# Performance work log

Measured on AMD Instinct MI355X. Metric: run time of the kernel, lower is better.

## Reference

```python
import jax, jax.numpy as jnp
import numpy as np

N, E = 40000, 640000
S_IN, V_IN = 64, 32            # input irreps: 64x0e + 32x1o (dim 160)
S_MID, V_MID = 96, 128         # tp output: (64+32)x0e, (64+32+32)x1o
S_OUT, V_OUT = 96, 32          # gate irreps_in: 64x0e scalars + 32x0e gates + 32x1o gated
R = 64                         # edge scalar (radial basis) dim
FC_HID = 64
W_NUMEL = 64 + 64 + 32 + 32 + 32  # per-edge tp weights ('uvu', v=1): 224
NUM_NEIGHBORS = 16.0


def setup_inputs() -> dict:
    key = jax.random.key(0)
    ks = jax.random.split(key, 13)
    return {
        "node_features": jax.random.normal(ks[0], (N, S_IN + 3 * V_IN), jnp.float32),
        "node_attr": jnp.ones((N, 1), jnp.float32),
        "edge_src": jax.random.randint(ks[1], (E,), 0, N),
        "edge_dst": jax.random.randint(ks[2], (E,), 0, N),
        "edge_attr": jax.random.normal(ks[3], (E, 4), jnp.float32),
        "edge_scalars": jax.random.normal(ks[4], (E, R), jnp.float32),
        "lin1_ws": jax.random.normal(ks[5], (S_IN, S_IN), jnp.float32),
        "lin1_wv": jax.random.normal(ks[6], (V_IN, V_IN), jnp.float32),
        "fc_w1": jax.random.normal(ks[7], (R, FC_HID), jnp.float32),
        "fc_w2": jax.random.normal(ks[8], (FC_HID, W_NUMEL), jnp.float32),
        "sc_ws": jax.random.normal(ks[9], (S_IN, S_OUT), jnp.float32),
        "sc_wv": jax.random.normal(ks[10], (V_IN, V_OUT), jnp.float32),
        "lin2_ws": jax.random.normal(ks[11], (S_MID, S_OUT), jnp.float32),
        "lin2_wv": jax.random.normal(ks[12], (V_MID, V_OUT), jnp.float32),
    }


def _inv(d):
    return 1.0 / jnp.sqrt(jnp.float32(d))


def _forward(node_features, node_attr, edge_attr, edge_scalars,
             lin1_ws, lin1_wv, fc_w1, fc_w2, sc_ws, sc_wv, lin2_ws, lin2_wv,
             edge_src, edge_dst):
    n = node_features.shape[0]
    s = node_features[:, :S_IN]                      # [N,64] 0e
    v = node_features[:, S_IN:].reshape(n, V_IN, 3)  # [N,32,3] 1o
    a = node_attr                                    # [N,1] scalar node attr

    # self-connection: FullyConnectedTensorProduct(input, 1x0e attr, out) == per-irrep linear
    sc_s = (s @ sc_ws) * a * _inv(S_IN)                                    # [N,96]
    sc_v = jnp.einsum('nci,cd->ndi', v, sc_wv) * a[:, :, None] * _inv(V_IN)  # [N,32,3]

    # lin1
    h_s = (s @ lin1_ws) * a * _inv(S_IN)
    h_v = jnp.einsum('nci,cd->ndi', v, lin1_wv) * a[:, :, None] * _inv(V_IN)

    # per-edge tensor-product weights from FC on edge scalars (silu MLP, no bias)
    hid = jax.nn.silu((edge_scalars @ fc_w1) * _inv(R))
    w = (hid @ fc_w2) * _inv(FC_HID)                 # [E,224]
    w1, w2, w3, w4, w5 = jnp.split(w, [64, 128, 160, 192], axis=-1)

    # gather source node features
    es = h_s[edge_src]                               # [E,64]
    ev = h_v[edge_src]                               # [E,32,3]
    e0 = edge_attr[:, :1]                            # [E,1]  0e
    e1 = edge_attr[:, 1:4]                           # [E,3]  1o

    # Clebsch-Gordan tensor product paths ('uvu', per-edge weights)
    m_s1 = w1 * es * e0                                                   # 0e x 0e -> 0e [E,64]
    m_s2 = w4 * jnp.einsum('eci,ei->ec', ev, e1) * _inv(3)                # 1o x 1o -> 0e [E,32]
    m_v1 = (w2 * es)[:, :, None] * e1[:, None, :]                         # 0e x 1o -> 1o [E,64,3]
    m_v2 = w3[:, :, None] * ev * e0[:, :, None]                           # 1o x 0e -> 1o [E,32,3]
    m_v3 = w5[:, :, None] * jnp.cross(ev, e1[:, None, :]) * _inv(2)       # 1o x 1o -> 1o [E,32,3]

    mid_s = jnp.concatenate([m_s1, m_s2], axis=-1)        # [E,96]
    mid_v = jnp.concatenate([m_v1, m_v2, m_v3], axis=1)   # [E,128,3]

    # scatter-sum to destination nodes, normalized by sqrt(num_neighbors)
    inv_nn = 1.0 / jnp.sqrt(jnp.float32(NUM_NEIGHBORS))
    agg_s = jax.ops.segment_sum(mid_s, edge_dst, num_segments=n) * inv_nn
    agg_v = jax.ops.segment_sum(mid_v, edge_dst, num_segments=n) * inv_nn

    # lin2
    o_s = (agg_s @ lin2_ws) * a * _inv(S_MID)                                  # [N,96]
    o_v = jnp.einsum('nci,cd->ndi', agg_v, lin2_wv) * a[:, :, None] * _inv(V_MID)  # [N,32,3]

    pre_s = sc_s + o_s
    pre_v = sc_v + o_v

    # Gate: silu on scalars, sigmoid gates multiply the l=1 features
    scalars = jax.nn.silu(pre_s[:, :64])
    gates = jax.nn.sigmoid(pre_s[:, 64:96])
    gated = gates[:, :, None] * pre_v                 # [N,32,3]
    return jnp.concatenate([scalars, gated.reshape(n, 3 * V_OUT)], axis=-1)  # [N,160]


def reference(node_features, node_attr, edge_src, edge_dst, edge_attr, edge_scalars,
              lin1_ws, lin1_wv, fc_w1, fc_w2, sc_ws, sc_wv, lin2_ws, lin2_wv):
    return _forward(node_features, node_attr, edge_attr, edge_scalars,
                    lin1_ws, lin1_wv, fc_w1, fc_w2, sc_ws, sc_wv, lin2_ws, lin2_wv,
                    edge_src, edge_dst)
```

## Files before the change

kernel.cpp:

```cpp
#include <hip/hip_runtime.h>

constexpr int N_NODES = 40000;
constexpr int N_EDGES = 640000;

constexpr float C_INV8     = 0.125f;
constexpr float C_INV_S32  = 0.17677669529663687f;
constexpr float C_INV_S3   = 0.57735026918962576f;
constexpr float C_INV_S2   = 0.70710678118654752f;
constexpr float C_INV_S96  = 0.10206207261596575f;
constexpr float C_INV_S128 = 0.08838834764831845f;
constexpr float C_INV_NN   = 0.25f;

typedef __attribute__((ext_vector_type(8))) short short8;
typedef __attribute__((ext_vector_type(4))) float f32x4;

__device__ __forceinline__ unsigned short f2bf(float x) {
  __bf16 b = (__bf16)x;
  return __builtin_bit_cast(unsigned short, b);
}
__device__ __forceinline__ float bf2f(unsigned short h) {
  return __uint_as_float(((unsigned int)h) << 16);
}

__global__ __launch_bounds__(256) void k_prep(
    const float* __restrict__ fc_w1, const float* __restrict__ fc_w2,
    const float* __restrict__ lin2_ws, const float* __restrict__ lin2_wv,
    unsigned short* __restrict__ w1t, unsigned short* __restrict__ w2t,
    unsigned short* __restrict__ wst, unsigned short* __restrict__ wvt)
{
  int t = blockIdx.x * 256 + threadIdx.x;
  if (t < 4096) {
    int c = t >> 6, k = t & 63;
    w1t[c * 64 + k] = f2bf(fc_w1[k * 64 + c]);
  } else if (t < 4096 + 14336) {
    int u = t - 4096; int c = u >> 6, k = u & 63;
    w2t[c * 64 + k] = f2bf(fc_w2[k * 224 + c]);
  } else if (t < 18432 + 9216) {
    int u = t - 18432; int c = u / 96, k = u - c * 96;
    wst[c * 96 + k] = f2bf(lin2_ws[k * 96 + c] * (C_INV_NN * C_INV_S96));
  } else if (t < 27648 + 4096) {
    int u = t - 27648; int d = u >> 7, k = u & 127;
    wvt[d * 128 + k] = f2bf(lin2_wv[k * 32 + d] * (C_INV_NN * C_INV_S128));
  }
}

__global__ __launch_bounds__(256) void k_node_hs(
    const float* __restrict__ nf, const float* __restrict__ attr,
    const float* __restrict__ w, float* __restrict__ h_s)
{
  int t = blockIdx.x * 256 + threadIdx.x;
  if (t >= N_NODES * 64) return;
  int n = t >> 6, c = t & 63;
  const float* s = nf + (long)n * 160;
  float acc = 0.f;
  #pragma unroll 8
  for (int k = 0; k < 64; ++k) acc = fmaf(s[k], w[k * 64 + c], acc);
  h_s[t] = acc * attr[n] * C_INV8;
}

__global__ __launch_bounds__(256) void k_node_hv(
    const float* __restrict__ nf, const float* __restrict__ attr,
    const float* __restrict__ w, float* __restrict__ h_v)
{
  int t = blockIdx.x * 256 + threadIdx.x;
  if (t >= N_NODES * 32) return;
  int n = t >> 5, d = t & 31;
  const float* v = nf + (long)n * 160 + 64;
  float a0 = 0.f, a1 = 0.f, a2 = 0.f;
  #pragma unroll 8
  for (int c = 0; c < 32; ++c) {
    float wv = w[c * 32 + d];
    a0 = fmaf(v[3 * c + 0], wv, a0);
    a1 = fmaf(v[3 * c + 1], wv, a1);
    a2 = fmaf(v[3 * c + 2], wv, a2);
  }
  float sc = attr[n] * C_INV_S32;
  h_v[(long)t * 3 + 0] = a0 * sc;
  h_v[(long)t * 3 + 1] = a1 * sc;
  h_v[(long)t * 3 + 2] = a2 * sc;
}

__global__ __launch_bounds__(256) void k_deg(const int* __restrict__ edst,
                                             int* __restrict__ deg)
{
  int e = blockIdx.x * 256 + threadIdx.x;
  if (e < N_EDGES) atomicAdd(&deg[edst[e]], 1);
}

__global__ __launch_bounds__(1024) void k_scan(const int* __restrict__ deg,
                                               int* __restrict__ start,
                                               int* __restrict__ cursor)
{
  __shared__ int psum[1024];
  int tid = threadIdx.x;
  const int PER = 40;
  int base = tid * PER;
  int s = 0;
  for (int i = 0; i < PER; ++i) {
    int idx = base + i;
    if (idx < N_NODES) s += deg[idx];
  }
  psum[tid] = s;
  __syncthreads();
  for (int off = 1; off < 1024; off <<= 1) {
    int v = psum[tid];
    int u = (tid >= off) ? psum[tid - off] : 0;
    __syncthreads();
    psum[tid] = v + u;
    __syncthreads();
  }
  int run = (tid == 0) ? 0 : psum[tid - 1];
  for (int i = 0; i < PER; ++i) {
    int idx = base + i;
    if (idx < N_NODES) {
      start[idx] = run; cursor[idx] = run;
      run += deg[idx];
    }
  }
  if (tid == 1023) start[N_NODES] = run;
}

__global__ __launch_bounds__(256) void k_fill(const int* __restrict__ edst,
                                              int* __restrict__ cursor,
                                              int* __restrict__ eid)
{
  int e = blockIdx.x * 256 + threadIdx.x;
  if (e < N_EDGES) {
    int p = atomicAdd(&cursor[edst[e]], 1);
    eid[p] = e;
  }
}

__global__ __launch_bounds__(256, 2) void k_edge2(
    const float* __restrict__ escal, const float* __restrict__ eattr,
    const int* __restrict__ esrc,
    const unsigned short* __restrict__ w1t, const unsigned short* __restrict__ w2t,
    const unsigned short* __restrict__ wst, const unsigned short* __restrict__ wvt,
    const float* __restrict__ h_s, const float* __restrict__ h_v,
    unsigned short* __restrict__ e_out)
{
  __shared__ unsigned short hid_lds[64 * 72];
  __shared__ unsigned short w_lds[64 * 232];
  int tid = threadIdx.x, warp = tid >> 6, lane = tid & 63;
  int lr = lane & 15, lg = lane >> 4;
  long e0 = (long)blockIdx.x * 64;
  int r0 = warp * 16;

  long eM = e0 + r0 + lr;
  int srcM = esrc[eM];
  float4 ea4 = *reinterpret_cast<const float4*>(eattr + eM * 4);
  float ea0 = ea4.x, e1x = ea4.y, e1y = ea4.z, e1z = ea4.w;
  float esv[16];
  {
    const float* hsr = h_s + (long)srcM * 64;
    *reinterpret_cast<float4*>(&esv[0])  = *reinterpret_cast<const float4*>(hsr + lg * 8);
    *reinterpret_cast<float4*>(&esv[4])  = *reinterpret_cast<const float4*>(hsr + lg * 8 + 4);
    *reinterpret_cast<float4*>(&esv[8])  = *reinterpret_cast<const float4*>(hsr + 32 + lg * 8);
    *reinterpret_cast<float4*>(&esv[12]) = *reinterpret_cast<const float4*>(hsr + 32 + lg * 8 + 4);
  }
  float evv[24];
  {
    const float* hvr = h_v + (long)srcM * 96 + lg * 24;
    #pragma unroll
    for (int q = 0; q < 6; ++q)
      *reinterpret_cast<float4*>(&evv[4 * q]) = *reinterpret_cast<const float4*>(hvr + 4 * q);
  }

  f32x4 acc[4] = {};
  #pragma unroll
  for (int ks = 0; ks < 2; ++ks) {
    const float* ap = escal + (e0 + r0 + lr) * 64 + ks * 32 + lg * 8;
    float4 a01 = *reinterpret_cast<const float4*>(ap);
    float4 a23 = *reinterpret_cast<const float4*>(ap + 4);
    short8 af;
    af[0] = (short)f2bf(a01.x); af[1] = (short)f2bf(a01.y);
    af[2] = (short)f2bf(a01.z); af[3] = (short)f2bf(a01.w);
    af[4] = (short)f2bf(a23.x); af[5] = (short)f2bf(a23.y);
    af[6] = (short)f2bf(a23.z); af[7] = (short)f2bf(a23.w);
    #pragma unroll
    for (int nt = 0; nt < 4; ++nt) {
      short8 bf = *reinterpret_cast<const short8*>(w1t + (nt * 16 + lr) * 64 + ks * 32 + lg * 8);
      acc[nt] = __builtin_amdgcn_mfma_f32_16x16x32_bf16(af, bf, acc[nt], 0, 0, 0);
    }
  }
  #pragma unroll
  for (int nt = 0; nt < 4; ++nt)
    #pragma unroll
    for (int r = 0; r < 4; ++r) {
      float x = acc[nt][r] * C_INV8;
      float h = x / (1.f + __expf(-x));
      hid_lds[(r0 + lg * 4 + r) * 72 + nt * 16 + lr] = f2bf(h);
    }

  f32x4 acc2[14] = {};
  #pragma unroll
  for (int ks = 0; ks < 2; ++ks) {
    short8 af = *reinterpret_cast<const short8*>(hid_lds + (r0 + lr) * 72 + ks * 32 + lg * 8);
    #pragma unroll
    for (int nt = 0; nt < 14; ++nt) {
      short8 bf = *reinterpret_cast<const short8*>(w2t + (nt * 16 + lr) * 64 + ks * 32 + lg * 8);
      acc2[nt] = __builtin_amdgcn_mfma_f32_16x16x32_bf16(af, bf, acc2[nt], 0, 0, 0);
    }
  }
  #pragma unroll
  for (int nt = 0; nt < 14; ++nt)
    #pragma unroll
    for (int r = 0; r < 4; ++r)
      w_lds[(r0 + lg * 4 + r) * 232 + nt * 16 + lr] = f2bf(acc2[nt][r] * C_INV8);

  const unsigned short* wrow = w_lds + (r0 + lr) * 232;
  short8 w1a = *reinterpret_cast<const short8*>(wrow + lg * 8);
  short8 w1b = *reinterpret_cast<const short8*>(wrow + 32 + lg * 8);
  short8 w2a = *reinterpret_cast<const short8*>(wrow + 64 + lg * 8);
  short8 w2b = *reinterpret_cast<const short8*>(wrow + 96 + lg * 8);
  short8 w3s = *reinterpret_cast<const short8*>(wrow + 128 + lg * 8);
  short8 w4s = *reinterpret_cast<const short8*>(wrow + 160 + lg * 8);
  short8 w5s = *reinterpret_cast<const short8*>(wrow + 192 + lg * 8);

  f32x4 accS[6] = {};
  {
    short8 aS;
    #pragma unroll
    for (int j = 0; j < 8; ++j) aS[j] = (short)f2bf(bf2f((unsigned short)w1a[j]) * esv[j] * ea0);
    #pragma unroll
    for (int nt = 0; nt < 6; ++nt) {
      short8 b = *reinterpret_cast<const short8*>(wst + (nt * 16 + lr) * 96 + lg * 8);
      accS[nt] = __builtin_amdgcn_mfma_f32_16x16x32_bf16(aS, b, accS[nt], 0, 0, 0);
    }
    #pragma unroll
    for (int j = 0; j < 8; ++j) aS[j] = (short)f2bf(bf2f((unsigned short)w1b[j]) * esv[8 + j] * ea0);
    #pragma unroll
    for (int nt = 0; nt < 6; ++nt) {
      short8 b = *reinterpret_cast<const short8*>(wst + (nt * 16 + lr) * 96 + 32 + lg * 8);
      accS[nt] = __builtin_amdgcn_mfma_f32_16x16x32_bf16(aS, b, accS[nt], 0, 0, 0);
    }
    #pragma unroll
    for (int j = 0; j < 8; ++j) {
      float dot = evv[3 * j] * e1x + evv[3 * j + 1] * e1y + evv[3 * j + 2] * e1z;
      aS[j] = (short)f2bf(bf2f((unsigned short)w4s[j]) * dot * C_INV_S3);
    }
    #pragma unroll
    for (int nt = 0; nt < 6; ++nt) {
      short8 b = *reinterpret_cast<const short8*>(wst + (nt * 16 + lr) * 96 + 64 + lg * 8);
      accS[nt] = __builtin_amdgcn_mfma_f32_16x16x32_bf16(aS, b, accS[nt], 0, 0, 0);
    }
  }

  f32x4 accV[6] = {};
  #pragma unroll
  for (int i = 0; i < 3; ++i) {
    float e1i = (i == 0) ? e1x : (i == 1) ? e1y : e1z;
    short8 aV;
    #pragma unroll
    for (int j = 0; j < 8; ++j) aV[j] = (short)f2bf(bf2f((unsigned short)w2a[j]) * esv[j] * e1i);
    #pragma unroll
    for (int nt = 0; nt < 2; ++nt) {
      short8 b = *reinterpret_cast<const short8*>(wvt + (nt * 16 + lr) * 128 + lg * 8);
      accV[i * 2 + nt] = __builtin_amdgcn_mfma_f32_16x16x32_bf16(aV, b, accV[i * 2 + nt], 0, 0, 0);
    }
    #pragma unroll
    for (int j = 0; j < 8; ++j) aV[j] = (short)f2bf(bf2f((unsigned short)w2b[j]) * esv[8 + j] * e1i);
    #pragma unroll
    for (int nt = 0; nt < 2; ++nt) {
      short8 b = *reinterpret_cast<const short8*>(wvt + (nt * 16 + lr) * 128 + 32 + lg * 8);
      accV[i * 2 + nt] = __builtin_amdgcn_mfma_f32_16x16x32_bf16(aV, b, accV[i * 2 + nt], 0, 0, 0);
    }
    #pragma unroll
    for (int j = 0; j < 8; ++j) aV[j] = (short)f2bf(bf2f((unsigned short)w3s[j]) * evv[3 * j + i] * ea0);
    #pragma unroll
    for (int nt = 0; nt < 2; ++nt) {
      short8 b = *reinterpret_cast<const short8*>(wvt + (nt * 16 + lr) * 128 + 64 + lg * 8);
      accV[i * 2 + nt] = __builtin_amdgcn_mfma_f32_16x16x32_bf16(aV, b, accV[i * 2 + nt], 0, 0, 0);
    }
    #pragma unroll
    for (int j = 0; j < 8; ++j) {
      float ex = evv[3 * j], ey = evv[3 * j + 1], ez = evv[3 * j + 2];
      float cr = (i == 0) ? (ey * e1z - ez * e1y)
               : (i == 1) ? (ez * e1x - ex * e1z)
                          : (ex * e1y - ey * e1x);
      aV[j] = (short)f2bf(bf2f((unsigned short)w5s[j]) * cr * C_INV_S2);
    }
    #pragma unroll
    for (int nt = 0; nt < 2; ++nt) {
      short8 b = *reinterpret_cast<const short8*>(wvt + (nt * 16 + lr) * 128 + 96 + lg * 8);
      accV[i * 2 + nt] = __builtin_amdgcn_mfma_f32_16x16x32_bf16(aV, b, accV[i * 2 + nt], 0, 0, 0);
    }
  }

  unsigned short* o_lds = w_lds;
  #pragma unroll
  for (int nt = 0; nt < 6; ++nt)
    #pragma unroll
    for (int r = 0; r < 4; ++r)
      o_lds[(r0 + lg * 4 + r) * 232 + nt * 16 + lr] = f2bf(accS[nt][r]);
  #pragma unroll
  for (int q = 0; q < 6; ++q) {
    int i = q >> 1, nt = q & 1;
    #pragma unroll
    for (int r = 0; r < 4; ++r)
      o_lds[(r0 + lg * 4 + r) * 232 + 96 + i * 32 + nt * 16 + lr] = f2bf(accV[q][r]);
  }

  #pragma unroll
  for (int c3 = 0; c3 < 6; ++c3) {
    int chunk = c3 * 64 + lane;
    int row = chunk / 24, col = chunk % 24;
    float4 v4 = *reinterpret_cast<const float4*>(o_lds + (r0 + row) * 232 + col * 8);
    *reinterpret_cast<float4*>(e_out + (e0 + r0 + row) * 192 + col * 8) = v4;
  }
}

__global__ __launch_bounds__(128) void k_agg(
    const int* __restrict__ start, const int* __restrict__ eid,
    const unsigned short* __restrict__ eo, float* __restrict__ agg)
{
  int n = blockIdx.x, tid = threadIdx.x;
  if (tid >= 96) return;
  int s0 = start[n], s1 = start[n + 1];
  float acc0 = 0.f, acc1 = 0.f;
  for (int base = s0; base < s1; base += 16) {
    int cnt = s1 - base; if (cnt > 16) cnt = 16;
    unsigned int vals[16];
    #pragma unroll
    for (int k = 0; k < 16; ++k) {
      int idx = base + k; if (idx > s1 - 1) idx = s1 - 1;
      int e = eid[idx];
      unsigned int v = *reinterpret_cast<const unsigned int*>(eo + (long)e * 192 + tid * 2);
      vals[k] = (k < cnt) ? v : 0u;
    }
    #pragma unroll
    for (int k = 0; k < 16; ++k) {
      acc0 += bf2f((unsigned short)(vals[k] & 0xffffu));
      acc1 += bf2f((unsigned short)(vals[k] >> 16));
    }
  }
  float2 o = make_float2(acc0, acc1);
  *reinterpret_cast<float2*>(agg + (long)n * 192 + tid * 2) = o;
}

__global__ __launch_bounds__(256) void k_fin_s(
    const float* __restrict__ nf, const float* __restrict__ attr,
    const float* __restrict__ agg, const float* __restrict__ sc_ws,
    float* __restrict__ out, float* __restrict__ gate)
{
  int t = blockIdx.x * 256 + threadIdx.x;
  if (t >= N_NODES * 96) return;
  int n = t / 96, cch = t - n * 96;
  const float* s = nf + (long)n * 160;
  float acc2 = 0.f;
  #pragma unroll 8
  for (int k = 0; k < 64; ++k) acc2 = fmaf(s[k], sc_ws[k * 96 + cch], acc2);
  float pre = (agg[(long)n * 192 + cch] + acc2 * C_INV8) * attr[n];
  if (cch < 64) out[(long)n * 160 + cch] = pre / (1.f + __expf(-pre));
  else gate[n * 32 + cch - 64] = 1.f / (1.f + __expf(-pre));
}

__global__ __launch_bounds__(256) void k_fin_v(
    const float* __restrict__ nf, const float* __restrict__ attr,
    const float* __restrict__ agg, const float* __restrict__ sc_wv,
    const float* __restrict__ gate, float* __restrict__ out)
{
  int t = blockIdx.x * 256 + threadIdx.x;
  if (t >= N_NODES * 32) return;
  int n = t >> 5, d = t & 31;
  const float* v = nf + (long)n * 160 + 64;
  float s0 = 0.f, s1 = 0.f, s2 = 0.f;
  #pragma unroll 8
  for (int cc = 0; cc < 32; ++cc) {
    float wv = sc_wv[cc * 32 + d];
    s0 = fmaf(v[3 * cc + 0], wv, s0);
    s1 = fmaf(v[3 * cc + 1], wv, s1);
    s2 = fmaf(v[3 * cc + 2], wv, s2);
  }
  const float* ag = agg + (long)n * 192 + 96;
  float a = attr[n];
  float g = gate[t];
  float p0 = (ag[0 * 32 + d] + s0 * C_INV_S32) * a;
  float p1 = (ag[1 * 32 + d] + s1 * C_INV_S32) * a;
  float p2 = (ag[2 * 32 + d] + s2 * C_INV_S32) * a;
  float* o = out + (long)n * 160 + 64 + 3 * d;
  o[0] = g * p0; o[1] = g * p1; o[2] = g * p2;
}

extern "C" void kernel_launch(void* const* d_in, const int* in_sizes, int n_in,
                              void* d_out, int out_size, void* d_ws, size_t ws_size,
                              hipStream_t stream)
{
  const float* nf      = (const float*)d_in[0];
  const float* attr    = (const float*)d_in[1];
  const int*   esrc    = (const int*)d_in[2];
  const int*   edst    = (const int*)d_in[3];
  const float* eattr   = (const float*)d_in[4];
  const float* escal   = (const float*)d_in[5];
  const float* lin1_ws = (const float*)d_in[6];
  const float* lin1_wv = (const float*)d_in[7];
  const float* fc_w1   = (const float*)d_in[8];
  const float* fc_w2   = (const float*)d_in[9];
  const float* sc_ws   = (const float*)d_in[10];
  const float* sc_wv   = (const float*)d_in[11];
  const float* lin2_ws = (const float*)d_in[12];
  const float* lin2_wv = (const float*)d_in[13];
  float* out = (float*)d_out;

  char* base = (char*)d_ws;
  size_t off = 0;
  auto carve = [&](size_t bytes) { void* p = base + off; off = (off + bytes + 63) & ~(size_t)63; return p; };
  float* h_s   = (float*)carve((size_t)N_NODES * 64 * 4);
  float* h_v   = (float*)carve((size_t)N_NODES * 96 * 4);
  float* agg   = (float*)carve((size_t)N_NODES * 192 * 4);
  unsigned short* w1t = (unsigned short*)carve(4096 * 2);
  unsigned short* w2t = (unsigned short*)carve(14336 * 2);
  unsigned short* wst = (unsigned short*)carve(9216 * 2);
  unsigned short* wvt = (unsigned short*)carve(4096 * 2);
  int* deg    = (int*)carve((size_t)N_NODES * 4);
  int* startp = (int*)carve((size_t)(N_NODES + 1) * 4);
  int* cursor = (int*)carve((size_t)N_NODES * 4);
  int* eid    = (int*)carve((size_t)N_EDGES * 4);
  unsigned short* e_out = (unsigned short*)carve((size_t)N_EDGES * 192 * 2);
  float* gate = h_s;

  k_prep<<<124, 256, 0, stream>>>(fc_w1, fc_w2, lin2_ws, lin2_wv, w1t, w2t, wst, wvt);
  k_node_hs<<<(N_NODES * 64 + 255) / 256, 256, 0, stream>>>(nf, attr, lin1_ws, h_s);
  k_node_hv<<<(N_NODES * 32 + 255) / 256, 256, 0, stream>>>(nf, attr, lin1_wv, h_v);

  hipMemsetAsync(deg, 0, (size_t)N_NODES * 4, stream);
  k_deg<<<(N_EDGES + 255) / 256, 256, 0, stream>>>(edst, deg);
  k_scan<<<1, 1024, 0, stream>>>(deg, startp, cursor);
  k_fill<<<(N_EDGES + 255) / 256, 256, 0, stream>>>(edst, cursor, eid);
  k_edge2<<<N_EDGES / 64, 256, 0, stream>>>(escal, eattr, esrc,
                                            w1t, w2t, wst, wvt, h_s, h_v, e_out);
  k_agg<<<N_NODES, 128, 0, stream>>>(startp, eid, e_out, agg);
  k_fin_s<<<(N_NODES * 96 + 255) / 256, 256, 0, stream>>>(nf, attr, agg, sc_ws, out, gate);
  k_fin_v<<<(N_NODES * 32 + 255) / 256, 256, 0, stream>>>(nf, attr, agg, sc_wv, gate, out);
}
```

Baseline: 704.6 us.

## Process edges in destination-sorted order so aggregation reads contiguous rows

The edge kernel now reads edges through the destination-sorted permutation and writes its outputs at the sorted position. The aggregation step can then stream contiguous rows per node with one thread per channel, instead of gathering through the edge-id indirection. The edge kernel also drops a separate LDS buffer by reusing the weight tile, which allows a higher occupancy hint, and the node and finalize kernels are each merged into one launch. The cost is that the edge kernel's input reads (scalars, attributes, source ids) become scattered gathers, and the gate pre-activation is recomputed inside the vector path.

```diff
diff --git a/kernel.cpp b/kernel.cpp
--- a/kernel.cpp
+++ b/kernel.cpp
@@ -44,40 +44,37 @@
   }
 }
 
-__global__ __launch_bounds__(256) void k_node_hs(
+__global__ __launch_bounds__(256) void k_node(
     const float* __restrict__ nf, const float* __restrict__ attr,
-    const float* __restrict__ w, float* __restrict__ h_s)
+    const float* __restrict__ ws_, const float* __restrict__ wv_,
+    float* __restrict__ h_s, float* __restrict__ h_v)
 {
   int t = blockIdx.x * 256 + threadIdx.x;
-  if (t >= N_NODES * 64) return;
-  int n = t >> 6, c = t & 63;
-  const float* s = nf + (long)n * 160;
-  float acc = 0.f;
-  #pragma unroll 8
-  for (int k = 0; k < 64; ++k) acc = fmaf(s[k], w[k * 64 + c], acc);
-  h_s[t] = acc * attr[n] * C_INV8;
-}
-
-__global__ __launch_bounds__(256) void k_node_hv(
-    const float* __restrict__ nf, const float* __restrict__ attr,
-    const float* __restrict__ w, float* __restrict__ h_v)
-{
-  int t = blockIdx.x * 256 + threadIdx.x;
-  if (t >= N_NODES * 32) return;
-  int n = t >> 5, d = t & 31;
-  const float* v = nf + (long)n * 160 + 64;
-  float a0 = 0.f, a1 = 0.f, a2 = 0.f;
-  #pragma unroll 8
-  for (int c = 0; c < 32; ++c) {
-    float wv = w[c * 32 + d];
-    a0 = fmaf(v[3 * c + 0], wv, a0);
-    a1 = fmaf(v[3 * c + 1], wv, a1);
-    a2 = fmaf(v[3 * c + 2], wv, a2);
-  }
-  float sc = attr[n] * C_INV_S32;
-  h_v[(long)t * 3 + 0] = a0 * sc;
-  h_v[(long)t * 3 + 1] = a1 * sc;
-  h_v[(long)t * 3 + 2] = a2 * sc;
+  if (t < N_NODES * 64) {
+    int n = t >> 6, c = t & 63;
+    const float* s = nf + (long)n * 160;
+    float acc = 0.f;
+    #pragma unroll 8
+    for (int k = 0; k < 64; ++k) acc = fmaf(s[k], ws_[k * 64 + c], acc);
+    h_s[t] = acc * attr[n] * C_INV8;
+  } else {
+    int u = t - N_NODES * 64;
+    if (u >= N_NODES * 32) return;
+    int n = u >> 5, d = u & 31;
+    const float* v = nf + (long)n * 160 + 64;
+    float a0 = 0.f, a1 = 0.f, a2 = 0.f;
+    #pragma unroll 8
+    for (int c = 0; c < 32; ++c) {
+      float wv = wv_[c * 32 + d];
+      a0 = fmaf(v[3 * c + 0], wv, a0);
+      a1 = fmaf(v[3 * c + 1], wv, a1);
+      a2 = fmaf(v[3 * c + 2], wv, a2);
+    }
+    float sc = attr[n] * C_INV_S32;
+    h_v[(long)u * 3 + 0] = a0 * sc;
+    h_v[(long)u * 3 + 1] = a1 * sc;
+    h_v[(long)u * 3 + 2] = a2 * sc;
+  }
 }
 
 __global__ __launch_bounds__(256) void k_deg(const int* __restrict__ edst,
@@ -131,24 +128,25 @@
   }
 }
 
-__global__ __launch_bounds__(256, 2) void k_edge2(
+__global__ __launch_bounds__(256, 5) void k_edge2(
     const float* __restrict__ escal, const float* __restrict__ eattr,
-    const int* __restrict__ esrc,
+    const int* __restrict__ esrc, const int* __restrict__ eid,
     const unsigned short* __restrict__ w1t, const unsigned short* __restrict__ w2t,
     const unsigned short* __restrict__ wst, const unsigned short* __restrict__ wvt,
     const float* __restrict__ h_s, const float* __restrict__ h_v,
     unsigned short* __restrict__ e_out)
 {
-  __shared__ unsigned short hid_lds[64 * 72];
   __shared__ unsigned short w_lds[64 * 232];
   int tid = threadIdx.x, warp = tid >> 6, lane = tid & 63;
   int lr = lane & 15, lg = lane >> 4;
   long e0 = (long)blockIdx.x * 64;
   int r0 = warp * 16;
-
-  long eM = e0 + r0 + lr;
-  int srcM = esrc[eM];
-  float4 ea4 = *reinterpret_cast<const float4*>(eattr + eM * 4);
+  unsigned short* wp = w_lds + r0 * 232;
+
+  long pos = e0 + r0 + lr;
+  int sid = eid[pos];
+  int srcM = esrc[sid];
+  float4 ea4 = *reinterpret_cast<const float4*>(eattr + (long)sid * 4);
   float ea0 = ea4.x, e1x = ea4.y, e1y = ea4.z, e1z = ea4.w;
   float esv[16];
   {
@@ -169,7 +167,7 @@
   f32x4 acc[4] = {};
   #pragma unroll
   for (int ks = 0; ks < 2; ++ks) {
-    const float* ap = escal + (e0 + r0 + lr) * 64 + ks * 32 + lg * 8;
+    const float* ap = escal + (long)sid * 64 + ks * 32 + lg * 8;
     float4 a01 = *reinterpret_cast<const float4*>(ap);
     float4 a23 = *reinterpret_cast<const float4*>(ap + 4);
     short8 af;
@@ -189,13 +187,13 @@
     for (int r = 0; r < 4; ++r) {
       float x = acc[nt][r] * C_INV8;
       float h = x / (1.f + __expf(-x));
-      hid_lds[(r0 + lg * 4 + r) * 72 + nt * 16 + lr] = f2bf(h);
+      wp[(lg * 4 + r) * 72 + nt * 16 + lr] = f2bf(h);
     }
 
   f32x4 acc2[14] = {};
   #pragma unroll
   for (int ks = 0; ks < 2; ++ks) {
-    short8 af = *reinterpret_cast<const short8*>(hid_lds + (r0 + lr) * 72 + ks * 32 + lg * 8);
+    short8 af = *reinterpret_cast<const short8*>(wp + lr * 72 + ks * 32 + lg * 8);
     #pragma unroll
     for (int nt = 0; nt < 14; ++nt) {
       short8 bf = *reinterpret_cast<const short8*>(w2t + (nt * 16 + lr) * 64 + ks * 32 + lg * 8);
@@ -206,9 +204,9 @@
   for (int nt = 0; nt < 14; ++nt)
     #pragma unroll
     for (int r = 0; r < 4; ++r)
-      w_lds[(r0 + lg * 4 + r) * 232 + nt * 16 + lr] = f2bf(acc2[nt][r] * C_INV8);
-
-  const unsigned short* wrow = w_lds + (r0 + lr) * 232;
+      wp[(lg * 4 + r) * 232 + nt * 16 + lr] = f2bf(acc2[nt][r] * C_INV8);
+
+  const unsigned short* wrow = wp + lr * 232;
   short8 w1a = *reinterpret_cast<const short8*>(wrow + lg * 8);
   short8 w1b = *reinterpret_cast<const short8*>(wrow + 32 + lg * 8);
   short8 w2a = *reinterpret_cast<const short8*>(wrow + 64 + lg * 8);
@@ -287,99 +285,102 @@
     }
   }
 
-  unsigned short* o_lds = w_lds;
   #pragma unroll
   for (int nt = 0; nt < 6; ++nt)
     #pragma unroll
     for (int r = 0; r < 4; ++r)
-      o_lds[(r0 + lg * 4 + r) * 232 + nt * 16 + lr] = f2bf(accS[nt][r]);
+      wp[(lg * 4 + r) * 232 + nt * 16 + lr] = f2bf(accS[nt][r]);
   #pragma unroll
   for (int q = 0; q < 6; ++q) {
     int i = q >> 1, nt = q & 1;
     #pragma unroll
     for (int r = 0; r < 4; ++r)
-      o_lds[(r0 + lg * 4 + r) * 232 + 96 + i * 32 + nt * 16 + lr] = f2bf(accV[q][r]);
+      wp[(lg * 4 + r) * 232 + 96 + i * 32 + nt * 16 + lr] = f2bf(accV[q][r]);
   }
 
   #pragma unroll
   for (int c3 = 0; c3 < 6; ++c3) {
     int chunk = c3 * 64 + lane;
     int row = chunk / 24, col = chunk % 24;
-    float4 v4 = *reinterpret_cast<const float4*>(o_lds + (r0 + row) * 232 + col * 8);
+    float4 v4 = *reinterpret_cast<const float4*>(wp + row * 232 + col * 8);
     *reinterpret_cast<float4*>(e_out + (e0 + r0 + row) * 192 + col * 8) = v4;
   }
 }
 
-__global__ __launch_bounds__(128) void k_agg(
-    const int* __restrict__ start, const int* __restrict__ eid,
-    const unsigned short* __restrict__ eo, float* __restrict__ agg)
-{
-  int n = blockIdx.x, tid = threadIdx.x;
-  if (tid >= 96) return;
+__global__ __launch_bounds__(256) void k_agg(
+    const int* __restrict__ start, const unsigned short* __restrict__ eo,
+    float* __restrict__ agg)
+{
+  int t = blockIdx.x * 256 + threadIdx.x;
+  if (t >= N_NODES * 96) return;
+  int n = t / 96, c = t - n * 96;
   int s0 = start[n], s1 = start[n + 1];
-  float acc0 = 0.f, acc1 = 0.f;
-  for (int base = s0; base < s1; base += 16) {
-    int cnt = s1 - base; if (cnt > 16) cnt = 16;
-    unsigned int vals[16];
-    #pragma unroll
-    for (int k = 0; k < 16; ++k) {
-      int idx = base + k; if (idx > s1 - 1) idx = s1 - 1;
-      int e = eid[idx];
-      unsigned int v = *reinterpret_cast<const unsigned int*>(eo + (long)e * 192 + tid * 2);
-      vals[k] = (k < cnt) ? v : 0u;
-    }
-    #pragma unroll
-    for (int k = 0; k < 16; ++k) {
-      acc0 += bf2f((unsigned short)(vals[k] & 0xffffu));
-      acc1 += bf2f((unsigned short)(vals[k] >> 16));
-    }
-  }
-  float2 o = make_float2(acc0, acc1);
-  *reinterpret_cast<float2*>(agg + (long)n * 192 + tid * 2) = o;
-}
-
-__global__ __launch_bounds__(256) void k_fin_s(
+  const unsigned int* base = reinterpret_cast<const unsigned int*>(eo);
+  float a0 = 0.f, a1 = 0.f;
+  long idx = (long)s0 * 96 + c;
+  int k = s0;
+  for (; k + 8 <= s1; k += 8) {
+    unsigned int v[8];
+    #pragma unroll
+    for (int j = 0; j < 8; ++j) v[j] = base[idx + (long)j * 96];
+    #pragma unroll
+    for (int j = 0; j < 8; ++j) {
+      a0 += bf2f((unsigned short)(v[j] & 0xffffu));
+      a1 += bf2f((unsigned short)(v[j] >> 16));
+    }
+    idx += 8 * 96;
+  }
+  for (; k < s1; ++k) {
+    unsigned int v = base[idx];
+    a0 += bf2f((unsigned short)(v & 0xffffu));
+    a1 += bf2f((unsigned short)(v >> 16));
+    idx += 96;
+  }
+  agg[(long)n * 192 + 2 * c]     = a0;
+  agg[(long)n * 192 + 2 * c + 1] = a1;
+}
+
+__global__ __launch_bounds__(256) void k_fin(
     const float* __restrict__ nf, const float* __restrict__ attr,
     const float* __restrict__ agg, const float* __restrict__ sc_ws,
-    float* __restrict__ out, float* __restrict__ gate)
+    const float* __restrict__ sc_wv, float* __restrict__ out)
 {
   int t = blockIdx.x * 256 + threadIdx.x;
-  if (t >= N_NODES * 96) return;
-  int n = t / 96, cch = t - n * 96;
-  const float* s = nf + (long)n * 160;
-  float acc2 = 0.f;
-  #pragma unroll 8
-  for (int k = 0; k < 64; ++k) acc2 = fmaf(s[k], sc_ws[k * 96 + cch], acc2);
-  float pre = (agg[(long)n * 192 + cch] + acc2 * C_INV8) * attr[n];
-  if (cch < 64) out[(long)n * 160 + cch] = pre / (1.f + __expf(-pre));
-  else gate[n * 32 + cch - 64] = 1.f / (1.f + __expf(-pre));
-}
-
-__global__ __launch_bounds__(256) void k_fin_v(
-    const float* __restrict__ nf, const float* __restrict__ attr,
-    const float* __restrict__ agg, const float* __restrict__ sc_wv,
-    const float* __restrict__ gate, float* __restrict__ out)
-{
-  int t = blockIdx.x * 256 + threadIdx.x;
-  if (t >= N_NODES * 32) return;
-  int n = t >> 5, d = t & 31;
-  const float* v = nf + (long)n * 160 + 64;
-  float s0 = 0.f, s1 = 0.f, s2 = 0.f;
-  #pragma unroll 8
-  for (int cc = 0; cc < 32; ++cc) {
-    float wv = sc_wv[cc * 32 + d];
-    s0 = fmaf(v[3 * cc + 0], wv, s0);
-    s1 = fmaf(v[3 * cc + 1], wv, s1);
-    s2 = fmaf(v[3 * cc + 2], wv, s2);
-  }
-  const float* ag = agg + (long)n * 192 + 96;
-  float a = attr[n];
-  float g = gate[t];
-  float p0 = (ag[0 * 32 + d] + s0 * C_INV_S32) * a;
-  float p1 = (ag[1 * 32 + d] + s1 * C_INV_S32) * a;
-  float p2 = (ag[2 * 32 + d] + s2 * C_INV_S32) * a;
-  float* o = out + (long)n * 160 + 64 + 3 * d;
-  o[0] = g * p0; o[1] = g * p1; o[2] = g * p2;
+  if (t < N_NODES * 64) {
+    int n = t >> 6, cch = t & 63;
+    const float* s = nf + (long)n * 160;
+    float acc2 = 0.f;
+    #pragma unroll 8
+    for (int k = 0; k < 64; ++k) acc2 = fmaf(s[k], sc_ws[k * 96 + cch], acc2);
+    float pre = (agg[(long)n * 192 + cch] + acc2 * C_INV8) * attr[n];
+    out[(long)n * 160 + cch] = pre / (1.f + __expf(-pre));
+  } else {
+    int u = t - N_NODES * 64;
+    if (u >= N_NODES * 32) return;
+    int n = u >> 5, d = u & 31;
+    const float* s = nf + (long)n * 160;
+    float a = attr[n];
+    float gacc = 0.f;
+    #pragma unroll 8
+    for (int k = 0; k < 64; ++k) gacc = fmaf(s[k], sc_ws[k * 96 + 64 + d], gacc);
+    float gpre = (agg[(long)n * 192 + 64 + d] + gacc * C_INV8) * a;
+    float g = 1.f / (1.f + __expf(-gpre));
+    const float* v = s + 64;
+    float s0 = 0.f, s1 = 0.f, s2 = 0.f;
+    #pragma unroll 8
+    for (int cc = 0; cc < 32; ++cc) {
+      float wv = sc_wv[cc * 32 + d];
+      s0 = fmaf(v[3 * cc + 0], wv, s0);
+      s1 = fmaf(v[3 * cc + 1], wv, s1);
+      s2 = fmaf(v[3 * cc + 2], wv, s2);
+    }
+    const float* ag = agg + (long)n * 192 + 96;
+    float p0 = (ag[d]      + s0 * C_INV_S32) * a;
+    float p1 = (ag[32 + d] + s1 * C_INV_S32) * a;
+    float p2 = (ag[64 + d] + s2 * C_INV_S32) * a;
+    float* o = out + (long)n * 160 + 64 + 3 * d;
+    o[0] = g * p0; o[1] = g * p1; o[2] = g * p2;
+  }
 }
 
 extern "C" void kernel_launch(void* const* d_in, const int* in_sizes, int n_in,
@@ -417,19 +418,16 @@
   int* cursor = (int*)carve((size_t)N_NODES * 4);
   int* eid    = (int*)carve((size_t)N_EDGES * 4);
   unsigned short* e_out = (unsigned short*)carve((size_t)N_EDGES * 192 * 2);
-  float* gate = h_s;
 
   k_prep<<<124, 256, 0, stream>>>(fc_w1, fc_w2, lin2_ws, lin2_wv, w1t, w2t, wst, wvt);
-  k_node_hs<<<(N_NODES * 64 + 255) / 256, 256, 0, stream>>>(nf, attr, lin1_ws, h_s);
-  k_node_hv<<<(N_NODES * 32 + 255) / 256, 256, 0, stream>>>(nf, attr, lin1_wv, h_v);
+  k_node<<<(N_NODES * 96 + 255) / 256, 256, 0, stream>>>(nf, attr, lin1_ws, lin1_wv, h_s, h_v);
 
   hipMemsetAsync(deg, 0, (size_t)N_NODES * 4, stream);
   k_deg<<<(N_EDGES + 255) / 256, 256, 0, stream>>>(edst, deg);
   k_scan<<<1, 1024, 0, stream>>>(deg, startp, cursor);
   k_fill<<<(N_EDGES + 255) / 256, 256, 0, stream>>>(edst, cursor, eid);
-  k_edge2<<<N_EDGES / 64, 256, 0, stream>>>(escal, eattr, esrc,
+  k_edge2<<<N_EDGES / 64, 256, 0, stream>>>(escal, eattr, esrc, eid,
                                             w1t, w2t, wst, wvt, h_s, h_v, e_out);
-  k_agg<<<N_NODES, 128, 0, stream>>>(startp, eid, e_out, agg);
-  k_fin_s<<<(N_NODES * 96 + 255) / 256, 256, 0, stream>>>(nf, attr, agg, sc_ws, out, gate);
-  k_fin_v<<<(N_NODES * 32 + 255) / 256, 256, 0, stream>>>(nf, attr, agg, sc_wv, gate, out);
-}
+  k_agg<<<(N_NODES * 96 + 255) / 256, 256, 0, stream>>>(startp, e_out, agg);
+  k_fin<<<(N_NODES * 96 + 255) / 256, 256, 0, stream>>>(nf, attr, agg, sc_ws, sc_wv, out);
+}
```

Measured after the change: 930.3 us. +32.0%, slower.
